# Kernel optimization log

Measured on AMD Instinct MI355X. Metric: run time of the kernel, lower is better.

Reference implementation:

```python
import jax, jax.numpy as jnp
import numpy as np
from jax import lax

DYADIC_ORDER = 0
NAIVE_SOLVER = False


def _increments(X, Y):
    # Linear static kernel Gram: (A, M, N)
    G = jnp.einsum('amd,and->amn', X, Y)
    # Second-order finite-difference increments: (A, M-1, N-1)
    inc = G[:, 1:, 1:] + G[:, :-1, :-1] - G[:, 1:, :-1] - G[:, :-1, 1:]
    f = 2 ** DYADIC_ORDER
    if f > 1:
        # torch `tile` with index_select == consecutive repeat == jnp.repeat
        inc = jnp.repeat(jnp.repeat(inc, f, axis=1), f, axis=2) / float(f * f)
    return inc


def _sig_kernel(X, Y):
    """Signature-kernel PDE solve. X:(A,M,D), Y:(A,N,D) -> (A,)"""
    inc = _increments(X, Y)            # (A, MM, NN)
    A, MM, NN = inc.shape

    def row_step(prev_row, g_row):
        # prev_row: (A, NN+1) = K[i, :];  g_row: (A, NN) = G[:, i, :]
        def col_step(k_left, inp):
            k00, k01, g = inp          # each (A,)
            if NAIVE_SOLVER:
                k_new = k_left + k01 + k00 * (g - 1.0)
            else:
                k_new = (k_left + k01) * (1.0 + 0.5 * g + g * g / 12.0) \
                        - k00 * (1.0 - g * g / 12.0)
            return k_new, k_new

        xs = (prev_row[:, :-1].T, prev_row[:, 1:].T, g_row.T)  # (NN, A) each
        _, tail = lax.scan(col_step, jnp.ones((A,), inc.dtype), xs)
        new_row = jnp.concatenate([jnp.ones((A, 1), inc.dtype), tail.T], axis=1)
        return new_row, None

    init_row = jnp.ones((A, NN + 1), inc.dtype)  # K[0, :] = 1
    final_row, _ = lax.scan(row_step, init_row, jnp.moveaxis(inc, 1, 0))
    return final_row[:, -1]            # K[:, MM, NN]


def setup_inputs() -> dict:
    key = jax.random.key(0)
    kx, ky = jax.random.split(key)
    A, M, D = 128, 256, 16
    # scale 0.1 keeps Gram increments small so the PDE stays stable
    X = 0.1 * jax.random.normal(kx, (A, M, D), dtype=jnp.float32)
    Y = 0.1 * jax.random.normal(ky, (A, M, D), dtype=jnp.float32)
    return {"X": X, "Y": Y}


def reference(X, Y):
    k_XX = _sig_kernel(X, X)
    k_YY = _sig_kernel(Y, Y)
    k_XY = _sig_kernel(X, Y)
    return jnp.mean(k_XX) + jnp.mean(k_YY) - 2.0 * jnp.mean(k_XY)
```

## Files before the change

### kernel.cpp

```cpp
#include <hip/hip_runtime.h>
#include <hip/hip_fp16.h>

typedef float f32x2 __attribute__((ext_vector_type(2)));

#define NA    128
#define NPTS  256
#define DD    16
#define MMI   255
#define NSTEP 318
#define RING  96

__device__ __forceinline__ float wave_shr1(float x, float boundary) {
    int r = __builtin_amdgcn_update_dpp(
        __builtin_bit_cast(int, boundary),
        __builtin_bit_cast(int, x),
        0x138 , 0xF, 0xF, false);
    return __builtin_bit_cast(float, r);
}

__global__ __launch_bounds__(256)
void sig_fused(const float* __restrict__ X, const float* __restrict__ Y,
               float* __restrict__ out) {
    const int pid  = blockIdx.x;
    const int pair = pid >> 7;
    const int a    = pid & 127;
    const float* U = (pair == 1) ? Y : X;
    const float* V = (pair == 0) ? X : Y;
    const float  w = (pair == 2) ? (-2.0f / (float)NA) : (1.0f / (float)NA);
    U += (size_t)a * (NPTS * DD);
    V += (size_t)a * (NPTS * DD);

    __shared__ float  dU[256][16];
    __shared__ __half ring[RING][256];

    const int tid  = threadIdx.x;
    const int wid  = tid >> 6;
    const int lane = tid & 63;

    {
        const float4* U4 = (const float4*)U;
        #pragma unroll
        for (int m = 0; m < 4; ++m) {
            int idx = tid + 256 * m;
            int row = idx >> 2;
            float4 val = make_float4(0.f, 0.f, 0.f, 0.f);
            if (row < MMI) {
                float4 lo = U4[idx];
                float4 hi = U4[idx + 4];
                val = make_float4(hi.x - lo.x, hi.y - lo.y,
                                  hi.z - lo.z, hi.w - lo.w);
            }
            *(float4*)(&dU[row][(idx & 3) * 4]) = val;
        }
    }
    {
        float4* rp = (float4*)&ring[0][0];
        const float4 z = make_float4(0.f, 0.f, 0.f, 0.f);
        #pragma unroll
        for (int m = 0; m < 12; ++m) rp[tid + 256 * m] = z;
    }

    f32x2 dv[4][8];
    if (wid != 0) {
        #pragma unroll
        for (int k = 0; k < 4; ++k) {
            int j = 4 * lane + k;
            const bool valid = (j < MMI);
            const int jj = valid ? j : 0;
            const float2* Va = (const float2*)(V + (size_t)jj * DD);
            const float2* Vb = (const float2*)(V + (size_t)(jj + 1) * DD);
            #pragma unroll
            for (int q = 0; q < 8; ++q) {
                float2 lo = Va[q], hi = Vb[q];
                dv[k][q] = valid ? f32x2{hi.x - lo.x, hi.y - lo.y}
                                 : f32x2{0.f, 0.f};
            }
        }
    }
    __syncthreads();

    auto produce = [&](int r) {
        int slot = r + lane;
        slot -= (slot >= 96)  ? 96 : 0;
        slot -= (slot >= 96)  ? 96 : 0;
        slot -= (slot >= 96)  ? 96 : 0;
        uint2 wv = make_uint2(0u, 0u);
        if (r < MMI) {
            const float4* up4 = (const float4*)&dU[r][0];
            float4 u0 = up4[0], u1 = up4[1], u2 = up4[2], u3 = up4[3];
            f32x2 uu[8] = {
                f32x2{u0.x, u0.y}, f32x2{u0.z, u0.w},
                f32x2{u1.x, u1.y}, f32x2{u1.z, u1.w},
                f32x2{u2.x, u2.y}, f32x2{u2.z, u2.w},
                f32x2{u3.x, u3.y}, f32x2{u3.z, u3.w}};
            f32x2 a0 = uu[0] * dv[0][0];
            f32x2 a1 = uu[0] * dv[1][0];
            f32x2 a2 = uu[0] * dv[2][0];
            f32x2 a3 = uu[0] * dv[3][0];
            #pragma unroll
            for (int q = 1; q < 8; ++q) {
                a0 = __builtin_elementwise_fma(uu[q], dv[0][q], a0);
                a1 = __builtin_elementwise_fma(uu[q], dv[1][q], a1);
                a2 = __builtin_elementwise_fma(uu[q], dv[2][q], a2);
                a3 = __builtin_elementwise_fma(uu[q], dv[3][q], a3);
            }
            __half2 h01 = __floats2half2_rn(a0.x + a0.y, a1.x + a1.y);
            __half2 h23 = __floats2half2_rn(a2.x + a2.y, a3.x + a3.y);
            wv.x = __builtin_bit_cast(unsigned int, h01);
            wv.y = __builtin_bit_cast(unsigned int, h23);
        }
        *(uint2*)(&ring[slot][4 * lane]) = wv;
    };

    float kup0 = 1.f, kup1 = 1.f, kup2 = 1.f, kup3 = 1.f;
    float shnew = 1.f, shprev = 1.f;

    auto STEP = [&](uint2 b) {
        float2 f01 = __half22float2(__builtin_bit_cast(__half2, b.x));
        float2 f23 = __half22float2(__builtin_bit_cast(__half2, b.y));
        f32x2 g01 = f32x2{f01.x, f01.y}, g23 = f32x2{f23.x, f23.y};
        f32x2 e01 = (g01 * g01) * f32x2{1.f/12.f, 1.f/12.f};
        f32x2 e23 = (g23 * g23) * f32x2{1.f/12.f, 1.f/12.f};
        f32x2 c1a = __builtin_elementwise_fma(g01, f32x2{0.5f, 0.5f},
                                              f32x2{1.f, 1.f}) + e01;
        f32x2 c1b = __builtin_elementwise_fma(g23, f32x2{0.5f, 0.5f},
                                              f32x2{1.f, 1.f}) + e23;
        f32x2 c2a = f32x2{1.f, 1.f} - e01;
        f32x2 c2b = f32x2{1.f, 1.f} - e23;
        const float left = shnew, upleft = shprev;
        const float pre0 = fmaf(kup0, c1a.x, -(upleft * c2a.x));
        const float pre1 = fmaf(kup1, c1a.y, -(kup0 * c2a.y));
        const float pre2 = fmaf(kup2, c1b.x, -(kup1 * c2b.x));
        const float pre3 = fmaf(kup3, c1b.y, -(kup2 * c2b.y));
        const float t0 = fmaf(left, c1a.x, pre0);
        const float t1 = fmaf(t0,   c1a.y, pre1);
        const float t2 = fmaf(t1,   c1b.x, pre2);
        const float t3 = fmaf(t2,   c1b.y, pre3);
        shprev = shnew;
        kup0 = t0; kup1 = t1; kup2 = t2; kup3 = t3;
        shnew = wave_shr1(t3, 1.0f);
    };

    if (wid != 0) {
        for (int i = wid - 1; i < 16; i += 3) produce(i);
    }
    __syncthreads();

    for (int ph = 0; ph < 19; ++ph) {
        if (wid == 0) {
            int slot0 = (16 * ph) % 96;
            uint2 gb[16];
            #pragma unroll
            for (int i = 0; i < 16; ++i) {
                int sl = slot0 + i;
                sl -= (sl >= 96) ? 96 : 0;
                gb[i] = *(const uint2*)(&ring[sl][4 * lane]);
            }
            #pragma unroll
            for (int i = 0; i < 16; ++i) STEP(gb[i]);
        } else {
            for (int i = wid - 1; i < 16; i += 3) {
                int r = 16 * ph + 16 + i;
                if (r < NSTEP) produce(r);
            }
        }
        __syncthreads();
    }

    if (wid == 0) {
        const int slot0 = 304 % 96;
        uint2 gb[14];
        #pragma unroll
        for (int i = 0; i < 14; ++i) {
            int sl = slot0 + i;
            sl -= (sl >= 96) ? 96 : 0;
            gb[i] = *(const uint2*)(&ring[sl][4 * lane]);
        }
        #pragma unroll
        for (int i = 0; i < 14; ++i) STEP(gb[i]);
        if (lane == 63) atomicAdd(out, w * kup2);
    }
}

extern "C" void kernel_launch(void* const* d_in, const int* in_sizes, int n_in,
                              void* d_out, int out_size, void* d_ws, size_t ws_size,
                              hipStream_t stream) {
    const float* X = (const float*)d_in[0];
    const float* Y = (const float*)d_in[1];
    float* out = (float*)d_out;
    hipMemsetAsync(out, 0, sizeof(float), stream);
    sig_fused<<<dim3(3 * NA), dim3(256), 0, stream>>>(X, Y, out);
}
```

Measured before the change: 100.2 us.

## Use fp16 dot2 for Gram increments, enlarge ring and phase size

Stores the U differences and the V differences as packed fp16 and computes the Gram increments with the fp16 dot2 instruction instead of fp32 packed FMAs. The ring buffer grows to 128 slots so the slot index becomes a cheap mask. The phase size doubles to 32 steps, halving the number of block barriers, and the consumer wave double-buffers its LDS loads across the steps. The intent is to cut producer ALU work and barrier overhead on the serial wavefront. In exchange, the inputs are now rounded to fp16 before the dot product, which loses precision, and the conversion uses round-toward-zero packing.

```diff
diff --git a/kernel.cpp b/kernel.cpp
--- a/kernel.cpp
+++ b/kernel.cpp
@@ -1,14 +1,16 @@
 #include <hip/hip_runtime.h>
 #include <hip/hip_fp16.h>
 
-typedef float f32x2 __attribute__((ext_vector_type(2)));
+typedef float    f32x2 __attribute__((ext_vector_type(2)));
+typedef _Float16 h16x2 __attribute__((ext_vector_type(2)));
 
 #define NA    128
 #define NPTS  256
 #define DD    16
 #define MMI   255
 #define NSTEP 318
-#define RING  96
+#define RINGN 128
+#define PH    32
 
 __device__ __forceinline__ float wave_shr1(float x, float boundary) {
     int r = __builtin_amdgcn_update_dpp(
@@ -16,6 +18,25 @@
         __builtin_bit_cast(int, x),
         0x138 , 0xF, 0xF, false);
     return __builtin_bit_cast(float, r);
+}
+
+__device__ __forceinline__ float fdot2h(unsigned int a, unsigned int b, float c) {
+#if __has_builtin(__builtin_amdgcn_fdot2)
+    return __builtin_amdgcn_fdot2(__builtin_bit_cast(h16x2, a),
+                                  __builtin_bit_cast(h16x2, b), c, false);
+#else
+    h16x2 ha = __builtin_bit_cast(h16x2, a), hb = __builtin_bit_cast(h16x2, b);
+    return c + (float)ha.x * (float)hb.x + (float)ha.y * (float)hb.y;
+#endif
+}
+
+__device__ __forceinline__ unsigned int pkh2(float a, float b) {
+#if __has_builtin(__builtin_amdgcn_cvt_pkrtz)
+    return __builtin_bit_cast(unsigned int, __builtin_amdgcn_cvt_pkrtz(a, b));
+#else
+    h16x2 h = {(_Float16)a, (_Float16)b};
+    return __builtin_bit_cast(unsigned int, h);
+#endif
 }
 
 __global__ __launch_bounds__(256)
@@ -30,41 +51,47 @@
     U += (size_t)a * (NPTS * DD);
     V += (size_t)a * (NPTS * DD);
 
-    __shared__ float  dU[256][16];
-    __shared__ __half ring[RING][256];
+    __shared__ unsigned short dUh[256][16];
+    __shared__ unsigned short ring[RINGN][256];
 
     const int tid  = threadIdx.x;
     const int wid  = tid >> 6;
     const int lane = tid & 63;
 
     {
-        const float4* U4 = (const float4*)U;
-        #pragma unroll
-        for (int m = 0; m < 4; ++m) {
-            int idx = tid + 256 * m;
-            int row = idx >> 2;
-            float4 val = make_float4(0.f, 0.f, 0.f, 0.f);
-            if (row < MMI) {
-                float4 lo = U4[idx];
-                float4 hi = U4[idx + 4];
-                val = make_float4(hi.x - lo.x, hi.y - lo.y,
-                                  hi.z - lo.z, hi.w - lo.w);
+        float du[16];
+        if (tid < MMI) {
+            const float4* Ua = (const float4*)(U + (size_t)tid * DD);
+            #pragma unroll
+            for (int q = 0; q < 4; ++q) {
+                float4 lo = Ua[q], hi = Ua[q + 4];
+                du[4*q+0] = hi.x - lo.x; du[4*q+1] = hi.y - lo.y;
+                du[4*q+2] = hi.z - lo.z; du[4*q+3] = hi.w - lo.w;
             }
-            *(float4*)(&dU[row][(idx & 3) * 4]) = val;
-        }
+        } else {
+            #pragma unroll
+            for (int k = 0; k < 16; ++k) du[k] = 0.f;
+        }
+        uint4 lo4, hi4;
+        lo4.x = pkh2(du[0],  du[1]);  lo4.y = pkh2(du[2],  du[3]);
+        lo4.z = pkh2(du[4],  du[5]);  lo4.w = pkh2(du[6],  du[7]);
+        hi4.x = pkh2(du[8],  du[9]);  hi4.y = pkh2(du[10], du[11]);
+        hi4.z = pkh2(du[12], du[13]); hi4.w = pkh2(du[14], du[15]);
+        *(uint4*)(&dUh[tid][0]) = lo4;
+        *(uint4*)(&dUh[tid][8]) = hi4;
     }
     {
-        float4* rp = (float4*)&ring[0][0];
-        const float4 z = make_float4(0.f, 0.f, 0.f, 0.f);
-        #pragma unroll
-        for (int m = 0; m < 12; ++m) rp[tid + 256 * m] = z;
-    }
-
-    f32x2 dv[4][8];
+        const uint4 z = {0u, 0u, 0u, 0u};
+        uint4* rp = (uint4*)&ring[0][0];
+        #pragma unroll
+        for (int m = 0; m < 16; ++m) rp[tid + 256*m] = z;
+    }
+
+    unsigned int dv2[4][8];
     if (wid != 0) {
         #pragma unroll
         for (int k = 0; k < 4; ++k) {
-            int j = 4 * lane + k;
+            int j = 4*lane + k;
             const bool valid = (j < MMI);
             const int jj = valid ? j : 0;
             const float2* Va = (const float2*)(V + (size_t)jj * DD);
@@ -72,44 +99,32 @@
             #pragma unroll
             for (int q = 0; q < 8; ++q) {
                 float2 lo = Va[q], hi = Vb[q];
-                dv[k][q] = valid ? f32x2{hi.x - lo.x, hi.y - lo.y}
-                                 : f32x2{0.f, 0.f};
+                float dx = valid ? hi.x - lo.x : 0.f;
+                float dy = valid ? hi.y - lo.y : 0.f;
+                dv2[k][q] = pkh2(dx, dy);
             }
         }
     }
     __syncthreads();
 
     auto produce = [&](int r) {
-        int slot = r + lane;
-        slot -= (slot >= 96)  ? 96 : 0;
-        slot -= (slot >= 96)  ? 96 : 0;
-        slot -= (slot >= 96)  ? 96 : 0;
         uint2 wv = make_uint2(0u, 0u);
         if (r < MMI) {
-            const float4* up4 = (const float4*)&dU[r][0];
-            float4 u0 = up4[0], u1 = up4[1], u2 = up4[2], u3 = up4[3];
-            f32x2 uu[8] = {
-                f32x2{u0.x, u0.y}, f32x2{u0.z, u0.w},
-                f32x2{u1.x, u1.y}, f32x2{u1.z, u1.w},
-                f32x2{u2.x, u2.y}, f32x2{u2.z, u2.w},
-                f32x2{u3.x, u3.y}, f32x2{u3.z, u3.w}};
-            f32x2 a0 = uu[0] * dv[0][0];
-            f32x2 a1 = uu[0] * dv[1][0];
-            f32x2 a2 = uu[0] * dv[2][0];
-            f32x2 a3 = uu[0] * dv[3][0];
-            #pragma unroll
-            for (int q = 1; q < 8; ++q) {
-                a0 = __builtin_elementwise_fma(uu[q], dv[0][q], a0);
-                a1 = __builtin_elementwise_fma(uu[q], dv[1][q], a1);
-                a2 = __builtin_elementwise_fma(uu[q], dv[2][q], a2);
-                a3 = __builtin_elementwise_fma(uu[q], dv[3][q], a3);
+            const uint2* du2 = (const uint2*)&dUh[r][0];
+            uint2 q0 = du2[0], q1 = du2[1], q2 = du2[2], q3 = du2[3];
+            unsigned int dh[8] = {q0.x, q0.y, q1.x, q1.y, q2.x, q2.y, q3.x, q3.y};
+            float a0 = 0.f, a1 = 0.f, a2 = 0.f, a3 = 0.f;
+            #pragma unroll
+            for (int q = 0; q < 8; ++q) {
+                a0 = fdot2h(dh[q], dv2[0][q], a0);
+                a1 = fdot2h(dh[q], dv2[1][q], a1);
+                a2 = fdot2h(dh[q], dv2[2][q], a2);
+                a3 = fdot2h(dh[q], dv2[3][q], a3);
             }
-            __half2 h01 = __floats2half2_rn(a0.x + a0.y, a1.x + a1.y);
-            __half2 h23 = __floats2half2_rn(a2.x + a2.y, a3.x + a3.y);
-            wv.x = __builtin_bit_cast(unsigned int, h01);
-            wv.y = __builtin_bit_cast(unsigned int, h23);
-        }
-        *(uint2*)(&ring[slot][4 * lane]) = wv;
+            wv.x = pkh2(a0, a1);
+            wv.y = pkh2(a2, a3);
+        }
+        *(uint2*)(&ring[(r + lane) & (RINGN - 1)][4*lane]) = wv;
     };
 
     float kup0 = 1.f, kup1 = 1.f, kup2 = 1.f, kup3 = 1.f;
@@ -141,43 +156,60 @@
         shnew = wave_shr1(t3, 1.0f);
     };
 
+    const unsigned short* rlane = &ring[0][4*lane];
+
     if (wid != 0) {
-        for (int i = wid - 1; i < 16; i += 3) produce(i);
+        for (int r = wid - 1; r < PH; r += 3) produce(r);
     }
     __syncthreads();
 
-    for (int ph = 0; ph < 19; ++ph) {
+    for (int ph = 0; ph < 9; ++ph) {
         if (wid == 0) {
-            int slot0 = (16 * ph) % 96;
-            uint2 gb[16];
-            #pragma unroll
-            for (int i = 0; i < 16; ++i) {
-                int sl = slot0 + i;
-                sl -= (sl >= 96) ? 96 : 0;
-                gb[i] = *(const uint2*)(&ring[sl][4 * lane]);
-            }
-            #pragma unroll
-            for (int i = 0; i < 16; ++i) STEP(gb[i]);
+            const unsigned short* rp = rlane + ((PH * ph) & (RINGN - 1)) * 256;
+            uint2 A[8], B[8];
+            #pragma unroll
+            for (int i = 0; i < 8; ++i) A[i] = *(const uint2*)(rp + i * 256);
+            #pragma unroll
+            for (int i = 0; i < 8; ++i) B[i] = *(const uint2*)(rp + (8 + i) * 256);
+            #pragma unroll
+            for (int i = 0; i < 8; ++i) STEP(A[i]);
+            #pragma unroll
+            for (int i = 0; i < 8; ++i) A[i] = *(const uint2*)(rp + (16 + i) * 256);
+            #pragma unroll
+            for (int i = 0; i < 8; ++i) STEP(B[i]);
+            #pragma unroll
+            for (int i = 0; i < 8; ++i) B[i] = *(const uint2*)(rp + (24 + i) * 256);
+            #pragma unroll
+            for (int i = 0; i < 8; ++i) STEP(A[i]);
+            #pragma unroll
+            for (int i = 0; i < 8; ++i) STEP(B[i]);
         } else {
-            for (int i = wid - 1; i < 16; i += 3) {
-                int r = 16 * ph + 16 + i;
-                if (r < NSTEP) produce(r);
-            }
+            int rend = PH * ph + 2 * PH;
+            if (rend > NSTEP) rend = NSTEP;
+            for (int r = PH * ph + PH + (wid - 1); r < rend; r += 3) produce(r);
         }
         __syncthreads();
     }
 
     if (wid == 0) {
-        const int slot0 = 304 % 96;
-        uint2 gb[14];
-        #pragma unroll
-        for (int i = 0; i < 14; ++i) {
-            int sl = slot0 + i;
-            sl -= (sl >= 96) ? 96 : 0;
-            gb[i] = *(const uint2*)(&ring[sl][4 * lane]);
-        }
-        #pragma unroll
-        for (int i = 0; i < 14; ++i) STEP(gb[i]);
+        const unsigned short* rp = rlane + ((PH * 9) & (RINGN - 1)) * 256;
+        uint2 A[8], B[8];
+        #pragma unroll
+        for (int i = 0; i < 8; ++i) A[i] = *(const uint2*)(rp + i * 256);
+        #pragma unroll
+        for (int i = 0; i < 8; ++i) B[i] = *(const uint2*)(rp + (8 + i) * 256);
+        #pragma unroll
+        for (int i = 0; i < 8; ++i) STEP(A[i]);
+        #pragma unroll
+        for (int i = 0; i < 8; ++i) A[i] = *(const uint2*)(rp + (16 + i) * 256);
+        #pragma unroll
+        for (int i = 0; i < 8; ++i) STEP(B[i]);
+        #pragma unroll
+        for (int i = 0; i < 6; ++i) B[i] = *(const uint2*)(rp + (24 + i) * 256);
+        #pragma unroll
+        for (int i = 0; i < 8; ++i) STEP(A[i]);
+        #pragma unroll
+        for (int i = 0; i < 6; ++i) STEP(B[i]);
         if (lane == 63) atomicAdd(out, w * kup2);
     }
 }
```

After: 91.09 us. 1.1x faster.

## Double-buffer ring loads into registers and widen ring to power-of-two pairs

Applied to the files above, without the earlier changes.

Changes the shared-memory ring to a 128-slot layout that interleaves pairs of rows per lane, so the consumer wave reads two rows with a single 16-byte load and wraps with a mask instead of conditional subtracts. The consumer now prefetches the next 16 rows into a second register buffer while stepping the current one, and producers run two phases ahead. It also switches the fp16 packing to the round-toward-zero convert intrinsic. The aim is to hide LDS latency on the serial recurrence wave, at the cost of more registers and a small rounding-mode change.

```diff
diff --git a/kernel.cpp b/kernel.cpp
--- a/kernel.cpp
+++ b/kernel.cpp
@@ -8,7 +8,9 @@
 #define DD    16
 #define MMI   255
 #define NSTEP 318
-#define RING  96
+#define RINGN 128
+#define NPAIR 64
+#define PH    16
 
 __device__ __forceinline__ float wave_shr1(float x, float boundary) {
     int r = __builtin_amdgcn_update_dpp(
@@ -16,6 +18,17 @@
         __builtin_bit_cast(int, x),
         0x138 , 0xF, 0xF, false);
     return __builtin_bit_cast(float, r);
+}
+
+__device__ __forceinline__ unsigned int pkh2(float a, float b) {
+#if __has_builtin(__builtin_amdgcn_cvt_pkrtz)
+    return __builtin_bit_cast(unsigned int, __builtin_amdgcn_cvt_pkrtz(a, b));
+#else
+    _Float16 x = (_Float16)a, y = (_Float16)b;
+    unsigned short lo = __builtin_bit_cast(unsigned short, x);
+    unsigned short hi = __builtin_bit_cast(unsigned short, y);
+    return (unsigned int)lo | ((unsigned int)hi << 16);
+#endif
 }
 
 __global__ __launch_bounds__(256)
@@ -30,41 +43,42 @@
     U += (size_t)a * (NPTS * DD);
     V += (size_t)a * (NPTS * DD);
 
-    __shared__ float  dU[256][16];
-    __shared__ __half ring[RING][256];
+    __shared__ float dU[256][16];
+    __shared__ uint2 ring2[NPAIR][64][2];
 
     const int tid  = threadIdx.x;
     const int wid  = tid >> 6;
     const int lane = tid & 63;
 
     {
-        const float4* U4 = (const float4*)U;
-        #pragma unroll
-        for (int m = 0; m < 4; ++m) {
-            int idx = tid + 256 * m;
-            int row = idx >> 2;
-            float4 val = make_float4(0.f, 0.f, 0.f, 0.f);
-            if (row < MMI) {
-                float4 lo = U4[idx];
-                float4 hi = U4[idx + 4];
-                val = make_float4(hi.x - lo.x, hi.y - lo.y,
-                                  hi.z - lo.z, hi.w - lo.w);
-            }
-            *(float4*)(&dU[row][(idx & 3) * 4]) = val;
+        float4 v0 = make_float4(0.f,0.f,0.f,0.f), v1 = v0, v2 = v0, v3 = v0;
+        if (tid < MMI) {
+            const float4* Ua = (const float4*)(U + (size_t)tid * DD);
+            float4 lo, hi;
+            lo = Ua[0]; hi = Ua[4];
+            v0 = make_float4(hi.x-lo.x, hi.y-lo.y, hi.z-lo.z, hi.w-lo.w);
+            lo = Ua[1]; hi = Ua[5];
+            v1 = make_float4(hi.x-lo.x, hi.y-lo.y, hi.z-lo.z, hi.w-lo.w);
+            lo = Ua[2]; hi = Ua[6];
+            v2 = make_float4(hi.x-lo.x, hi.y-lo.y, hi.z-lo.z, hi.w-lo.w);
+            lo = Ua[3]; hi = Ua[7];
+            v3 = make_float4(hi.x-lo.x, hi.y-lo.y, hi.z-lo.z, hi.w-lo.w);
         }
+        float4* dp = (float4*)&dU[tid][0];
+        dp[0] = v0; dp[1] = v1; dp[2] = v2; dp[3] = v3;
     }
     {
-        float4* rp = (float4*)&ring[0][0];
-        const float4 z = make_float4(0.f, 0.f, 0.f, 0.f);
-        #pragma unroll
-        for (int m = 0; m < 12; ++m) rp[tid + 256 * m] = z;
+        const uint4 z = {0u, 0u, 0u, 0u};
+        uint4* rp = (uint4*)&ring2[0][0][0];
+        #pragma unroll
+        for (int m = 0; m < 16; ++m) rp[tid + 256*m] = z;
     }
 
     f32x2 dv[4][8];
     if (wid != 0) {
         #pragma unroll
         for (int k = 0; k < 4; ++k) {
-            int j = 4 * lane + k;
+            int j = 4*lane + k;
             const bool valid = (j < MMI);
             const int jj = valid ? j : 0;
             const float2* Va = (const float2*)(V + (size_t)jj * DD);
@@ -80,23 +94,18 @@
     __syncthreads();
 
     auto produce = [&](int r) {
-        int slot = r + lane;
-        slot -= (slot >= 96)  ? 96 : 0;
-        slot -= (slot >= 96)  ? 96 : 0;
-        slot -= (slot >= 96)  ? 96 : 0;
+        int slot = (r + lane) & (RINGN - 1);
         uint2 wv = make_uint2(0u, 0u);
         if (r < MMI) {
-            const float4* up4 = (const float4*)&dU[r][0];
-            float4 u0 = up4[0], u1 = up4[1], u2 = up4[2], u3 = up4[3];
+            const float4* up = (const float4*)&dU[r][0];
+            float4 u0 = up[0], u1 = up[1], u2 = up[2], u3 = up[3];
             f32x2 uu[8] = {
-                f32x2{u0.x, u0.y}, f32x2{u0.z, u0.w},
-                f32x2{u1.x, u1.y}, f32x2{u1.z, u1.w},
-                f32x2{u2.x, u2.y}, f32x2{u2.z, u2.w},
-                f32x2{u3.x, u3.y}, f32x2{u3.z, u3.w}};
-            f32x2 a0 = uu[0] * dv[0][0];
-            f32x2 a1 = uu[0] * dv[1][0];
-            f32x2 a2 = uu[0] * dv[2][0];
-            f32x2 a3 = uu[0] * dv[3][0];
+                f32x2{u0.x,u0.y}, f32x2{u0.z,u0.w},
+                f32x2{u1.x,u1.y}, f32x2{u1.z,u1.w},
+                f32x2{u2.x,u2.y}, f32x2{u2.z,u2.w},
+                f32x2{u3.x,u3.y}, f32x2{u3.z,u3.w}};
+            f32x2 a0 = uu[0]*dv[0][0], a1 = uu[0]*dv[1][0];
+            f32x2 a2 = uu[0]*dv[2][0], a3 = uu[0]*dv[3][0];
             #pragma unroll
             for (int q = 1; q < 8; ++q) {
                 a0 = __builtin_elementwise_fma(uu[q], dv[0][q], a0);
@@ -104,20 +113,22 @@
                 a2 = __builtin_elementwise_fma(uu[q], dv[2][q], a2);
                 a3 = __builtin_elementwise_fma(uu[q], dv[3][q], a3);
             }
-            __half2 h01 = __floats2half2_rn(a0.x + a0.y, a1.x + a1.y);
-            __half2 h23 = __floats2half2_rn(a2.x + a2.y, a3.x + a3.y);
-            wv.x = __builtin_bit_cast(unsigned int, h01);
-            wv.y = __builtin_bit_cast(unsigned int, h23);
+            wv.x = pkh2(a0.x + a0.y, a1.x + a1.y);
+            wv.y = pkh2(a2.x + a2.y, a3.x + a3.y);
         }
-        *(uint2*)(&ring[slot][4 * lane]) = wv;
+        ring2[slot >> 1][lane][slot & 1] = wv;
+    };
+    auto produce_range = [&](int rb) {
+        int re = rb + PH; if (re > NSTEP) re = NSTEP;
+        for (int r = rb + wid - 1; r < re; r += 3) produce(r);
     };
 
     float kup0 = 1.f, kup1 = 1.f, kup2 = 1.f, kup3 = 1.f;
     float shnew = 1.f, shprev = 1.f;
 
-    auto STEP = [&](uint2 b) {
-        float2 f01 = __half22float2(__builtin_bit_cast(__half2, b.x));
-        float2 f23 = __half22float2(__builtin_bit_cast(__half2, b.y));
+    auto STEP = [&](unsigned int bx, unsigned int by) {
+        float2 f01 = __half22float2(__builtin_bit_cast(__half2, bx));
+        float2 f23 = __half22float2(__builtin_bit_cast(__half2, by));
         f32x2 g01 = f32x2{f01.x, f01.y}, g23 = f32x2{f23.x, f23.y};
         f32x2 e01 = (g01 * g01) * f32x2{1.f/12.f, 1.f/12.f};
         f32x2 e23 = (g23 * g23) * f32x2{1.f/12.f, 1.f/12.f};
@@ -141,43 +152,40 @@
         shnew = wave_shr1(t3, 1.0f);
     };
 
+    const char* rbase = (const char*)&ring2[0][lane][0];
+    auto LOADP = [&](int pb, uint4* dst) {
+        const char* p = rbase + (size_t)pb * 1024;
+        #pragma unroll
+        for (int i = 0; i < 8; ++i) dst[i] = *(const uint4*)(p + i * 1024);
+    };
+    auto STEP16 = [&](const uint4* c) {
+        #pragma unroll
+        for (int i = 0; i < 8; ++i) { STEP(c[i].x, c[i].y); STEP(c[i].z, c[i].w); }
+    };
+
     if (wid != 0) {
-        for (int i = wid - 1; i < 16; i += 3) produce(i);
+        for (int r = wid - 1; r < 2 * PH; r += 3) produce(r);
     }
     __syncthreads();
 
-    for (int ph = 0; ph < 19; ++ph) {
-        if (wid == 0) {
-            int slot0 = (16 * ph) % 96;
-            uint2 gb[16];
-            #pragma unroll
-            for (int i = 0; i < 16; ++i) {
-                int sl = slot0 + i;
-                sl -= (sl >= 96) ? 96 : 0;
-                gb[i] = *(const uint2*)(&ring[sl][4 * lane]);
-            }
-            #pragma unroll
-            for (int i = 0; i < 16; ++i) STEP(gb[i]);
-        } else {
-            for (int i = wid - 1; i < 16; i += 3) {
-                int r = 16 * ph + 16 + i;
-                if (r < NSTEP) produce(r);
-            }
-        }
+    uint4 A[8], B[8];
+    if (wid == 0) LOADP(0, A);
+
+    for (int h = 0; h < 9; ++h) {
+        const int q0 = 2 * h, q1 = 2 * h + 1;
+        if (wid == 0) { LOADP((8*q0 + 8) & 63, B); STEP16(A); }
+        else          produce_range(16*q0 + 32);
         __syncthreads();
-    }
-
+        if (wid == 0) { LOADP((8*q1 + 8) & 63, A); STEP16(B); }
+        else          produce_range(16*q1 + 32);
+        __syncthreads();
+    }
+    if (wid == 0) { LOADP((8*18 + 8) & 63, B); STEP16(A); }
+    else          produce_range(16*18 + 32);
+    __syncthreads();
     if (wid == 0) {
-        const int slot0 = 304 % 96;
-        uint2 gb[14];
-        #pragma unroll
-        for (int i = 0; i < 14; ++i) {
-            int sl = slot0 + i;
-            sl -= (sl >= 96) ? 96 : 0;
-            gb[i] = *(const uint2*)(&ring[sl][4 * lane]);
-        }
-        #pragma unroll
-        for (int i = 0; i < 14; ++i) STEP(gb[i]);
+        #pragma unroll
+        for (int i = 0; i < 7; ++i) { STEP(B[i].x, B[i].y); STEP(B[i].z, B[i].w); }
         if (lane == 63) atomicAdd(out, w * kup2);
     }
 }
```

After: 97.15 us. 1.03x faster.
